# Kernel tuning notes

Measured on AMD Instinct MI355X. Metric: run time of the kernel, lower is better.

## Reference

```python
import jax, jax.numpy as jnp
import numpy as np

B, T, E = 8, 1024, 512
H = 1024            # hidden_dim
NH, QD, VD = 4, 256, 512
C1, C2 = 512, 2     # conv1_out, conv2_out
K, PAD = 3, 1


def conv1d(x, w, b, pad):
    # x: [B, Cin, T], w: [Cout, Cin, K]
    y = jax.lax.conv_general_dilated(x, w, (1,), [(pad, pad)],
                                     dimension_numbers=('NCH', 'OIH', 'NCH'))
    return y + b[None, :, None]


def setup_inputs() -> dict:
    key = jax.random.key(0)
    ks = jax.random.split(key, 24)
    n = lambda i, shape, s=0.02: jax.random.normal(ks[i], shape, dtype=jnp.float32) * s
    inp = {
        'x':    jax.random.normal(ks[0], (B, T, E), dtype=jnp.float32),
        # in_pro: two 1x1 convs over channels (acting as linears)
        'w_in1': n(1, (E, E)), 'b_in1': jnp.zeros((E,), jnp.float32),
        'w_in2': n(2, (E, E)), 'b_in2': jnp.zeros((E,), jnp.float32),
        # attention projections
        'w_q': n(3, (NH * QD, E), float(np.sqrt(2.0 / (E + QD)))), 'b_q': jnp.zeros((NH * QD,), jnp.float32),
        'w_k': n(4, (NH * QD, E), float(np.sqrt(2.0 / (E + QD)))), 'b_k': jnp.zeros((NH * QD,), jnp.float32),
        'w_v': n(5, (NH * VD, E), float(np.sqrt(2.0 / (E + VD)))), 'b_v': jnp.zeros((NH * VD,), jnp.float32),
        # output projection (1x1 conv)
        'w_p': n(6, (E, NH * VD)), 'b_p': jnp.zeros((E,), jnp.float32),
        # layernorm
        'ln_g': jnp.ones((E,), jnp.float32), 'ln_b': jnp.zeros((E,), jnp.float32),
        # LSTM (1 layer, unidirectional, hidden H)
        'w_ih': n(7, (4 * H, E)), 'w_hh': n(8, (4 * H, H)),
        'b_ih': jnp.zeros((4 * H,), jnp.float32), 'b_hh': jnp.zeros((4 * H,), jnp.float32),
        # attention pooling convs
        'w_c1': n(9, (C1, H, K)), 'b_c1': jnp.zeros((C1,), jnp.float32),
        'w_c2': n(10, (C2, C1, K)), 'b_c2': jnp.zeros((C2,), jnp.float32),
    }
    return inp


def reference(x, w_in1, b_in1, w_in2, b_in2, w_q, b_q, w_k, b_k, w_v, b_v,
              w_p, b_p, ln_g, ln_b, w_ih, w_hh, b_ih, b_hh,
              w_c1, b_c1, w_c2, b_c2):
    # in_pro: 1x1 conv -> LeakyReLU(0.25) -> 1x1 conv (channel-wise linears)
    h = jnp.einsum('bte,fe->btf', x, w_in1) + b_in1
    h = jnp.where(h >= 0, h, 0.25 * h)
    h = jnp.einsum('bte,fe->btf', h, w_in2) + b_in2  # [B,T,E]

    # multi-head attention (no scale factor, as in the source)
    q = (jnp.einsum('bte,fe->btf', h, w_q) + b_q).reshape(B, T, NH, QD)
    k = (jnp.einsum('bte,fe->btf', h, w_k) + b_k).reshape(B, T, NH, QD)
    v = (jnp.einsum('bte,fe->btf', h, w_v) + b_v).reshape(B, T, NH, VD)
    scores = jnp.einsum('btnd,bsnd->bnts', q, k)          # [B,NH,T,T]
    attn = jax.nn.softmax(scores, axis=-1)
    o = jnp.einsum('bnts,bsnd->btnd', attn, v)            # [B,T,NH,VD]
    o = o.reshape(B, T, NH * VD)

    # p_conv1 (1x1) then LayerNorm over E
    y = jnp.einsum('btc,ec->bte', o, w_p) + b_p           # [B,T,E]
    mu = jnp.mean(y, axis=-1, keepdims=True)
    var = jnp.mean(jnp.square(y - mu), axis=-1, keepdims=True)
    y = (y - mu) * jax.lax.rsqrt(var + 1e-5) * ln_g + ln_b

    # LSTM (batch_first, 1 layer); dropout is identity in eval mode
    def step(carry, xt):
        hprev, cprev = carry
        g = xt @ w_ih.T + hprev @ w_hh.T + b_ih + b_hh    # [B,4H]
        i, f, gg, og = jnp.split(g, 4, axis=-1)
        c = jax.nn.sigmoid(f) * cprev + jax.nn.sigmoid(i) * jnp.tanh(gg)
        hn = jax.nn.sigmoid(og) * jnp.tanh(c)
        return (hn, c), hn
    init = (jnp.zeros((B, H), y.dtype), jnp.zeros((B, H), y.dtype))
    _, hs = jax.lax.scan(step, init, jnp.swapaxes(y, 0, 1))  # [T,B,H]
    lstm_out = jnp.swapaxes(hs, 0, 1)                        # [B,T,H]

    # conv-based attention pooling
    a = conv1d(jnp.swapaxes(lstm_out, 1, 2), w_c1, b_c1, PAD)  # [B,C1,T]
    a = jax.nn.relu(a)
    a = conv1d(a, w_c2, b_c2, PAD)                              # [B,C2,T]
    a = jax.nn.softmax(a, axis=2)
    feat = jnp.einsum('bct,bth->bch', a, lstm_out)              # [B,C2,H]
    return feat.reshape(B, C2 * H)
```

## Files before the change

kernel.cpp:

```cpp
#include <hip/hip_runtime.h>
#include <stdint.h>

typedef short short8 __attribute__((ext_vector_type(8)));
typedef short short4v __attribute__((ext_vector_type(4)));
typedef float float4v __attribute__((ext_vector_type(4)));

__device__ __forceinline__ float b2f(short s) {
    return __uint_as_float(((unsigned)(unsigned short)s) << 16);
}
__device__ __forceinline__ short f2b(float f) {
    unsigned u = __float_as_uint(f);
    unsigned r = (u + 0x7fffu + ((u >> 16) & 1u)) >> 16;
    return (short)r;
}

__global__ void k_f32_to_bf16(const float4v* __restrict__ in, short4v* __restrict__ out, int n4) {
    int i = blockIdx.x * blockDim.x + threadIdx.x;
    int stride = gridDim.x * blockDim.x;
    for (; i < n4; i += stride) {
        float4v v = in[i];
        short4v o;
        o[0] = f2b(v[0]); o[1] = f2b(v[1]); o[2] = f2b(v[2]); o[3] = f2b(v[3]);
        out[i] = o;
    }
}

__global__ void k_cvt_weights(const float4v* __restrict__ s0, const float4v* __restrict__ s1,
                              const float4v* __restrict__ s2, const float4v* __restrict__ s3,
                              const float4v* __restrict__ s4, const float4v* __restrict__ s5,
                              const float4v* __restrict__ s6, const float4v* __restrict__ s7,
                              short4v* __restrict__ dst) {
    int i = blockIdx.x * blockDim.x + threadIdx.x;
    int stride = gridDim.x * blockDim.x;
    for (; i < 2490368; i += stride) {
        float4v v;
        if      (i <   65536) v = s0[i];
        else if (i <  131072) v = s1[i -   65536];
        else if (i <  262144) v = s2[i -  131072];
        else if (i <  393216) v = s3[i -  262144];
        else if (i <  655360) v = s4[i -  393216];
        else if (i <  917504) v = s5[i -  655360];
        else if (i < 1441792) v = s6[i -  917504];
        else                  v = s7[i - 1441792];
        short4v o;
        o[0] = f2b(v[0]); o[1] = f2b(v[1]); o[2] = f2b(v[2]); o[3] = f2b(v[3]);
        dst[i] = o;
    }
}

__global__ void k_wc1_tr(const float* __restrict__ in, short* __restrict__ out) {
    int i = blockIdx.x * blockDim.x + threadIdx.x;
    if (i >= 512 * 3072) return;
    int c = i / 3072, rr = i % 3072, dk = rr / 1024, h = rr % 1024;
    out[i] = f2b(in[(c * 1024 + h) * 3 + dk]);
}

__global__ void k_bias_sum(const float* __restrict__ a, const float* __restrict__ b,
                           float* __restrict__ o, int n) {
    int i = blockIdx.x * blockDim.x + threadIdx.x;
    if (i < n) o[i] = a[i] + b[i];
}

__global__ __launch_bounds__(256) void k_gemm_bt(
    const short* __restrict__ A, const short* __restrict__ B,
    float* __restrict__ Cf, short* __restrict__ Cb,
    const float* __restrict__ bias,
    int M, int N, int K, int lda, int ldb, int ldc,
    int z0n, long sA0, long sA1, long sB0, long sB1, long sC0, long sC1,
    int act, int gap)
{
    __shared__ __align__(16) short lds[2 * 128 * 32];
    const int z = blockIdx.z;
    const int z0 = z % z0n, z1 = z / z0n;
    A += z1 * sA1 + z0 * sA0;
    B += z1 * sB1 + z0 * sB0;
    const long coff = z1 * sC1 + z0 * sC0;
    const int tn0 = blockIdx.x * 128, tm0 = blockIdx.y * 128;
    const int tid = threadIdx.x, ln = tid & 63, wv = tid >> 6;
    const int wr = wv >> 1, wc = wv & 1;

    const short* gbase[4];
    {
        const int gcol = (ln & 3) ^ ((ln >> 3) & 3);
#pragma unroll
        for (int j = 0; j < 4; ++j) {
            int c = wv * 4 + j;
            if (c < 8) {
                long grow = (long)(tm0 + c * 16 + (ln >> 2));
                if (gap) grow += 2 * (grow >> 10);
                gbase[j] = A + grow * (long)lda + gcol * 8;
            } else {
                gbase[j] = B + (long)(tn0 + (c - 8) * 16 + (ln >> 2)) * ldb + gcol * 8;
            }
        }
    }

    float4v acc[4][4];
#pragma unroll
    for (int i = 0; i < 4; ++i)
#pragma unroll
        for (int j = 0; j < 4; ++j) acc[i][j] = (float4v){0.f, 0.f, 0.f, 0.f};

    const int nk = K >> 5;
    for (int kt = 0; kt < nk; ++kt) {
        __syncthreads();
#pragma unroll
        for (int j = 0; j < 4; ++j) {
            int c = wv * 4 + j;
            __builtin_amdgcn_global_load_lds(
                (const __attribute__((address_space(1))) void*)(gbase[j] + kt * 32),
                (__attribute__((address_space(3))) void*)((short8*)lds + c * 64),
                16, 0, 0);
        }
        __syncthreads();

        short8 af[4], bf_[4];
        const int q = ln >> 4;
#pragma unroll
        for (int i = 0; i < 4; ++i) {
            int r = wr * 64 + i * 16 + (ln & 15);
            af[i] = ((short8*)lds)[r * 4 + (q ^ ((r >> 1) & 3))];
        }
#pragma unroll
        for (int j = 0; j < 4; ++j) {
            int r = wc * 64 + j * 16 + (ln & 15);
            bf_[j] = ((short8*)lds)[512 + r * 4 + (q ^ ((r >> 1) & 3))];
        }
#pragma unroll
        for (int i = 0; i < 4; ++i)
#pragma unroll
            for (int j = 0; j < 4; ++j)
                acc[i][j] = __builtin_amdgcn_mfma_f32_16x16x32_bf16(af[i], bf_[j], acc[i][j], 0, 0, 0);
    }

#pragma unroll
    for (int j = 0; j < 4; ++j) {
        int nglob = tn0 + wc * 64 + j * 16 + (ln & 15);
        float bv = bias ? bias[nglob] : 0.f;
#pragma unroll
        for (int i = 0; i < 4; ++i) {
#pragma unroll
            for (int r = 0; r < 4; ++r) {
                int mglob = tm0 + wr * 64 + i * 16 + (ln >> 4) * 4 + r;
                float v = acc[i][j][r] + bv;
                if (act == 1) v = (v >= 0.f) ? v : 0.25f * v;
                else if (act == 2) v = fmaxf(v, 0.f);
                long ci = coff + (long)mglob * ldc + nglob;
                if (Cf) Cf[ci] = v;
                if (Cb) Cb[ci] = f2b(v);
            }
        }
    }
}

__global__ __launch_bounds__(256) void k_softmax_rows_bf16(short* __restrict__ p) {
    long row = blockIdx.x;
    short* r = p + (row << 10);
    int tid = threadIdx.x;
    float v[4];
    float mx = -3.4e38f;
#pragma unroll
    for (int i = 0; i < 4; ++i) { v[i] = b2f(r[tid + (i << 8)]); mx = fmaxf(mx, v[i]); }
#pragma unroll
    for (int d = 32; d > 0; d >>= 1) mx = fmaxf(mx, __shfl_down(mx, d));
    __shared__ float red[4], red2[4];
    if ((tid & 63) == 0) red[tid >> 6] = mx;
    __syncthreads();
    mx = fmaxf(fmaxf(red[0], red[1]), fmaxf(red[2], red[3]));
    float s = 0.f;
#pragma unroll
    for (int i = 0; i < 4; ++i) { v[i] = expf(v[i] - mx); s += v[i]; }
#pragma unroll
    for (int d = 32; d > 0; d >>= 1) s += __shfl_down(s, d);
    if ((tid & 63) == 0) red2[tid >> 6] = s;
    __syncthreads();
    s = red2[0] + red2[1] + red2[2] + red2[3];
    float inv = 1.f / s;
#pragma unroll
    for (int i = 0; i < 4; ++i) r[tid + (i << 8)] = f2b(v[i] * inv);
}

__global__ __launch_bounds__(256) void k_layernorm(const short* __restrict__ y,
                                                   const float* __restrict__ gam,
                                                   const float* __restrict__ bet,
                                                   short* __restrict__ o) {
    const long row = blockIdx.x;
    const short* r = y + (row << 9);
    const int tid = threadIdx.x;
    float v0 = b2f(r[tid]), v1 = b2f(r[tid + 256]);
    float s = v0 + v1, ss = v0 * v0 + v1 * v1;
#pragma unroll
    for (int d = 32; d > 0; d >>= 1) { s += __shfl_down(s, d); ss += __shfl_down(ss, d); }
    __shared__ float rs_[4], rss[4];
    if ((tid & 63) == 0) { rs_[tid >> 6] = s; rss[tid >> 6] = ss; }
    __syncthreads();
    s = rs_[0] + rs_[1] + rs_[2] + rs_[3];
    ss = rss[0] + rss[1] + rss[2] + rss[3];
    float mean = s * (1.f / 512.f);
    float var = ss * (1.f / 512.f) - mean * mean;
    float rstd = rsqrtf(var + 1e-5f);
    short* out = o + (row << 9);
    out[tid]       = f2b((v0 - mean) * rstd * gam[tid]       + bet[tid]);
    out[tid + 256] = f2b((v1 - mean) * rstd * gam[tid + 256] + bet[tid + 256]);
}

__global__ __launch_bounds__(256) void k_vT(const short* __restrict__ v, short* __restrict__ vT) {
    __shared__ short t[32][34];
    int bn = blockIdx.z, b = bn >> 2, n = bn & 3;
    int s0 = blockIdx.y * 32, d0 = blockIdx.x * 32;
    int lx = threadIdx.x & 31, ly = threadIdx.x >> 5;
#pragma unroll
    for (int i = 0; i < 4; ++i) {
        int s = ly + i * 8;
        t[s][lx] = v[(long)(b * 1024 + s0 + s) * 2048 + n * 512 + d0 + lx];
    }
    __syncthreads();
#pragma unroll
    for (int i = 0; i < 4; ++i) {
        int d = ly + i * 8;
        vT[((long)bn * 512 + d0 + d) * 1024 + s0 + lx] = t[lx][d];
    }
}

__global__ __launch_bounds__(256) void k_lstm(
    const short* __restrict__ whh, const short* __restrict__ igb,
    short* __restrict__ hA, short* __restrict__ hB,
    short* __restrict__ lstm_pad, int* __restrict__ arr)
{
    const int g = blockIdx.x;
    const int tid = threadIdx.x;
    const int ln = tid & 63, wv = tid >> 6;
    const int kbase = wv * 256 + ((ln >> 4) << 3);
    const int arow = ln & 15;

    short8 wf[4][8];
#pragma unroll
    for (int q = 0; q < 4; ++q) {
        long row = (long)q * 1024 + g * 16 + (ln & 15);
#pragma unroll
        for (int kk = 0; kk < 8; ++kk)
            wf[q][kk] = *(const short8*)&whh[row * 1024 + kbase + kk * 32];
    }

    __shared__ float part[4][16][68];
    const int gm = tid >> 4, gu = tid & 15;
    float c_prev = 0.f;
    float igv[4];
    if (tid < 128) {
#pragma unroll
        for (int q = 0; q < 4; ++q)
            igv[q] = b2f(igb[((long)gm * 1024 + 0) * 4096 + q * 1024 + g * 16 + gu]);
    }

    for (int step = 0; step < 1024; ++step) {
        const short* hp = (step & 1) ? hB : hA;
        short8 af[8];
        if (arow < 8) {
            const unsigned long long* hq =
                (const unsigned long long*)(hp + arow * 1024 + kbase);
#pragma unroll
            for (int kk = 0; kk < 8; ++kk) {
                union { unsigned long long u[2]; short8 s; } cv;
                cv.u[0] = __hip_atomic_load(hq + kk * 8,     __ATOMIC_RELAXED, __HIP_MEMORY_SCOPE_AGENT);
                cv.u[1] = __hip_atomic_load(hq + kk * 8 + 1, __ATOMIC_RELAXED, __HIP_MEMORY_SCOPE_AGENT);
                af[kk] = cv.s;
            }
        } else {
#pragma unroll
            for (int kk = 0; kk < 8; ++kk) af[kk] = (short8){0, 0, 0, 0, 0, 0, 0, 0};
        }

        float4v acc[4];
#pragma unroll
        for (int q = 0; q < 4; ++q) acc[q] = (float4v){0.f, 0.f, 0.f, 0.f};
#pragma unroll
        for (int kk = 0; kk < 8; ++kk)
#pragma unroll
            for (int q = 0; q < 4; ++q)
                acc[q] = __builtin_amdgcn_mfma_f32_16x16x32_bf16(af[kk], wf[q][kk], acc[q], 0, 0, 0);

#pragma unroll
        for (int q = 0; q < 4; ++q)
#pragma unroll
            for (int rr = 0; rr < 4; ++rr)
                part[wv][(ln >> 4) * 4 + rr][q * 16 + (ln & 15)] = acc[q][rr];
        __syncthreads();

        if (tid < 128) {
            float psum[4];
#pragma unroll
            for (int q = 0; q < 4; ++q)
                psum[q] = part[0][gm][q * 16 + gu] + part[1][gm][q * 16 + gu]
                        + part[2][gm][q * 16 + gu] + part[3][gm][q * 16 + gu];
            float g0 = psum[0] + igv[0];
            float g1 = psum[1] + igv[1];
            float g2 = psum[2] + igv[2];
            float g3 = psum[3] + igv[3];
            float iv = 1.f / (1.f + __expf(-g0));
            float fv = 1.f / (1.f + __expf(-g1));
            float gv = 2.f / (1.f + __expf(-2.f * g2)) - 1.f;
            float ov = 1.f / (1.f + __expf(-g3));
            float c = fv * c_prev + iv * gv;
            c_prev = c;
            float h = ov * (2.f / (1.f + __expf(-2.f * c)) - 1.f);
            short hb16 = f2b(h);
            short* hn = (step & 1) ? hA : hB;
            __hip_atomic_store(&hn[gm * 1024 + g * 16 + gu], hb16,
                               __ATOMIC_RELAXED, __HIP_MEMORY_SCOPE_AGENT);
            lstm_pad[((long)gm * 1026 + step + 1) * 1024 + g * 16 + gu] = hb16;
        }

        __syncthreads();
        if (tid == 0)
            __hip_atomic_store(&arr[g], step + 1, __ATOMIC_RELAXED, __HIP_MEMORY_SCOPE_AGENT);
        if (tid < 128 && step + 1 < 1024) {
#pragma unroll
            for (int q = 0; q < 4; ++q)
                igv[q] = b2f(igb[((long)gm * 1024 + step + 1) * 4096 + q * 1024 + g * 16 + gu]);
        }
        if (wv == 0) {
            const int target = step + 1;
            long att = 0;
            while (true) {
                int f0 = __hip_atomic_load(&arr[ln], __ATOMIC_RELAXED, __HIP_MEMORY_SCOPE_AGENT);
                if (__all(f0 >= target)) break;
                if (++att > 20000000L) break;
                __builtin_amdgcn_s_sleep(1);
            }
        }
        __syncthreads();
    }
}

__global__ __launch_bounds__(256) void k_conv2(const short* __restrict__ a1,
                                               const float* __restrict__ w,
                                               const float* __restrict__ bias,
                                               float* __restrict__ a2) {
    __shared__ float wl[1536];
    int blk = blockIdx.x;
    int b = blk >> 3, c = (blk >> 2) & 1, t0 = (blk & 3) * 256;
    int tid = threadIdx.x;
    for (int i = tid; i < 1536; i += 256) wl[i] = w[c * 1536 + i];
    __syncthreads();
    int t = t0 + tid;
    float s = bias[c];
    for (int dk = 0; dk < 3; ++dk) {
        int tt = t + dk - 1;
        if (tt < 0 || tt >= 1024) continue;
        const short8* arow = (const short8*)(a1 + (long)(b * 1024 + tt) * 512);
        for (int j = 0; j < 64; ++j) {
            short8 v = arow[j];
#pragma unroll
            for (int u = 0; u < 8; ++u)
                s += b2f(v[u]) * wl[(j * 8 + u) * 3 + dk];
        }
    }
    a2[(b * 2 + c) * 1024 + t] = s;
}

__global__ __launch_bounds__(256) void k_feat(const float* __restrict__ a2,
                                              const short* __restrict__ lstm_pad,
                                              float* __restrict__ out) {
    int blk = blockIdx.x;
    int bc = blk >> 2, qh = blk & 3;
    int b = bc >> 1;
    int tid = threadIdx.x;
    int h = qh * 256 + tid;
    __shared__ float aw[1024];
    __shared__ float red[4], red2[4];
    float v[4];
    float mx = -3.4e38f;
#pragma unroll
    for (int i = 0; i < 4; ++i) { v[i] = a2[bc * 1024 + tid + (i << 8)]; mx = fmaxf(mx, v[i]); }
#pragma unroll
    for (int d = 32; d > 0; d >>= 1) mx = fmaxf(mx, __shfl_down(mx, d));
    if ((tid & 63) == 0) red[tid >> 6] = mx;
    __syncthreads();
    mx = fmaxf(fmaxf(red[0], red[1]), fmaxf(red[2], red[3]));
    float s = 0.f;
#pragma unroll
    for (int i = 0; i < 4; ++i) { v[i] = __expf(v[i] - mx); s += v[i]; }
#pragma unroll
    for (int d = 32; d > 0; d >>= 1) s += __shfl_down(s, d);
    if ((tid & 63) == 0) red2[tid >> 6] = s;
    __syncthreads();
    s = red2[0] + red2[1] + red2[2] + red2[3];
    float inv = 1.f / s;
#pragma unroll
    for (int i = 0; i < 4; ++i) aw[tid + (i << 8)] = v[i] * inv;
    __syncthreads();
    float acc = 0.f;
#pragma unroll 4
    for (int t = 0; t < 1024; ++t)
        acc += aw[t] * b2f(lstm_pad[((long)(b * 1026 + t + 1)) * 1024 + h]);
    out[bc * 1024 + h] = acc;
}

static void gemm_bt(hipStream_t st, const short* A, const short* B, float* Cf, short* Cb,
                    const float* bias, int M, int N, int K, int lda, int ldb, int ldc,
                    int z, int z0n, long sA0, long sA1, long sB0, long sB1, long sC0, long sC1,
                    int act, int gap) {
    dim3 grid(N / 128, M / 128, z);
    k_gemm_bt<<<grid, dim3(256), 0, st>>>(A, B, Cf, Cb, bias, M, N, K, lda, ldb, ldc,
                                          z0n, sA0, sA1, sB0, sB1, sC0, sC1, act, gap);
}

extern "C" void kernel_launch(void* const* d_in, const int* in_sizes, int n_in,
                              void* d_out, int out_size, void* d_ws, size_t ws_size,
                              hipStream_t stream) {
    if (ws_size < 199409920u) return;

    const float* x     = (const float*)d_in[0];
    const float* w_in1 = (const float*)d_in[1];
    const float* b_in1 = (const float*)d_in[2];
    const float* w_in2 = (const float*)d_in[3];
    const float* b_in2 = (const float*)d_in[4];
    const float* w_q   = (const float*)d_in[5];
    const float* b_q   = (const float*)d_in[6];
    const float* w_k   = (const float*)d_in[7];
    const float* b_k   = (const float*)d_in[8];
    const float* w_v   = (const float*)d_in[9];
    const float* b_v   = (const float*)d_in[10];
    const float* w_p   = (const float*)d_in[11];
    const float* b_p   = (const float*)d_in[12];
    const float* ln_g  = (const float*)d_in[13];
    const float* ln_b  = (const float*)d_in[14];
    const float* w_ih  = (const float*)d_in[15];
    const float* w_hh  = (const float*)d_in[16];
    const float* b_ih  = (const float*)d_in[17];
    const float* b_hh  = (const float*)d_in[18];
    const float* w_c1  = (const float*)d_in[19];
    const float* b_c1  = (const float*)d_in[20];
    const float* w_c2  = (const float*)d_in[21];
    const float* b_c2  = (const float*)d_in[22];

    char* ws = (char*)d_ws;
    short* w1b  = (short*)(ws + 0);
    short* w2b  = (short*)(ws + 524288);
    short* wqb  = (short*)(ws + 1048576);
    short* wkb  = (short*)(ws + 2097152);
    short* wvb  = (short*)(ws + 3145728);
    short* wpb  = (short*)(ws + 5242880);
    short* wihb = (short*)(ws + 7340032);
    short* whhb = (short*)(ws + 11534336);
    short* wc1b = (short*)(ws + 19922944);
    float* bsum = (float*)(ws + 23068672);
    short* hs0  = (short*)(ws + 23085056);
    short* hs1  = (short*)(ws + 23117824);
    int*   arr  = (int*)  (ws + 23150592);
    float* a2   = (float*)(ws + 23150848);
    short* lpad = (short*)(ws + 23216384);
    const size_t D0 = 40026368u;
    short* xbf   = (short*)(ws + D0);
    short* h1bf  = (short*)(ws + D0 + 8388608);
    short* h2bf  = (short*)(ws + D0 + 16777216);
    short* qbf   = (short*)(ws + D0 + 25165824);
    short* kbf   = (short*)(ws + D0 + 41943040);
    short* vbf   = (short*)(ws + D0 + 58720256);
    short* vTbf  = (short*)(ws + D0 + 92274688);
    short* scb   = (short*)(ws + D0 + 58720256);
    short* obf   = (short*)(ws + D0 + 125829120);
    short* ybf   = (short*)(ws + D0 + 58720256);
    short* ylnbf = (short*)(ws + D0 + 67108864);
    short* igb   = (short*)(ws + D0 + 92274688);
    short* a1bf  = (short*)(ws + D0);

    hipMemsetAsync(lpad, 0, (size_t)8 * 1026 * 1024 * 2, stream);
    hipMemsetAsync(hs0, 0, 32768, stream);
    hipMemsetAsync(hs1, 0, 32768, stream);
    hipMemsetAsync(arr, 0, 512, stream);

    k_f32_to_bf16<<<dim3(4096), dim3(256), 0, stream>>>((const float4v*)x, (short4v*)xbf, 1048576);
    k_cvt_weights<<<dim3(4096), dim3(256), 0, stream>>>(
        (const float4v*)w_in1, (const float4v*)w_in2, (const float4v*)w_q, (const float4v*)w_k,
        (const float4v*)w_v, (const float4v*)w_p, (const float4v*)w_ih, (const float4v*)w_hh,
        (short4v*)w1b);
    k_wc1_tr<<<dim3((512 * 3072 + 255) / 256), dim3(256), 0, stream>>>(w_c1, wc1b);
    k_bias_sum<<<dim3(16), dim3(256), 0, stream>>>(b_ih, b_hh, bsum, 4096);

    gemm_bt(stream, xbf, w1b, nullptr, h1bf, b_in1, 8192, 512, 512, 512, 512, 512,
            1, 1, 0, 0, 0, 0, 0, 0, 1, 0);
    gemm_bt(stream, h1bf, w2b, nullptr, h2bf, b_in2, 8192, 512, 512, 512, 512, 512,
            1, 1, 0, 0, 0, 0, 0, 0, 0, 0);
    gemm_bt(stream, h2bf, wqb, nullptr, qbf, b_q, 8192, 1024, 512, 512, 512, 1024,
            1, 1, 0, 0, 0, 0, 0, 0, 0, 0);
    gemm_bt(stream, h2bf, wkb, nullptr, kbf, b_k, 8192, 1024, 512, 512, 512, 1024,
            1, 1, 0, 0, 0, 0, 0, 0, 0, 0);
    gemm_bt(stream, h2bf, wvb, nullptr, vbf, b_v, 8192, 2048, 512, 512, 512, 2048,
            1, 1, 0, 0, 0, 0, 0, 0, 0, 0);
    k_vT<<<dim3(16, 32, 32), dim3(256), 0, stream>>>(vbf, vTbf);

    for (int bg = 0; bg < 2; ++bg) {
        const short* qb = qbf + (long)bg * 4194304;
        const short* kb = kbf + (long)bg * 4194304;
        gemm_bt(stream, qb, kb, nullptr, scb, nullptr, 1024, 1024, 256, 1024, 1024, 1024,
                16, 4, 256, 1048576, 256, 1048576, 1048576, 4194304, 0, 0);
        k_softmax_rows_bf16<<<dim3(16384), dim3(256), 0, stream>>>(scb);
        gemm_bt(stream, scb, vTbf + (long)bg * 8388608, nullptr, obf + (long)bg * 8388608, nullptr,
                1024, 512, 1024, 1024, 1024, 2048,
                16, 4, 1048576, 4194304, 524288, 2097152, 512, 2097152, 0, 0);
    }

    gemm_bt(stream, obf, wpb, nullptr, ybf, b_p, 8192, 512, 2048, 2048, 2048, 512,
            1, 1, 0, 0, 0, 0, 0, 0, 0, 0);
    k_layernorm<<<dim3(8192), dim3(256), 0, stream>>>(ybf, ln_g, ln_b, ylnbf);
    gemm_bt(stream, ylnbf, wihb, nullptr, igb, bsum, 8192, 4096, 512, 512, 512, 4096,
            1, 1, 0, 0, 0, 0, 0, 0, 0, 0);
    k_lstm<<<dim3(64), dim3(256), 0, stream>>>(whhb, igb, hs0, hs1, lpad, arr);
    gemm_bt(stream, lpad, wc1b, nullptr, a1bf, b_c1, 8192, 512, 3072, 1024, 3072, 512,
            1, 1, 0, 0, 0, 0, 0, 0, 2, 1);
    k_conv2<<<dim3(64), dim3(256), 0, stream>>>(a1bf, w_c2, b_c2, a2);
    k_feat<<<dim3(64), dim3(256), 0, stream>>>(a2, lpad, (float*)d_out);
    (void)in_sizes; (void)n_in; (void)out_size; (void)ws_size;
}
```

Before: 4.042 ms.

## Replace LSTM cross-block flag barrier with step-tagged hidden-state words

The persistent LSTM kernel previously published the hidden state, ran a block barrier, set a per-block arrival flag, and spun until all 64 flags reached the step. Each bf16 hidden value is now stored in a 32-bit word together with a 16-bit step tag. Consumers poll the hidden-state loads directly until every tag matches, which removes the arrival array, one __syncthreads, and the separate flag spin per step. This doubles the hidden-state buffer traffic and makes every wave spin on wider atomic loads without sleeping, which adds memory pressure while blocks wait.

```diff
diff --git a/kernel.cpp b/kernel.cpp
--- a/kernel.cpp
+++ b/kernel.cpp
@@ -224,8 +224,8 @@
 
 __global__ __launch_bounds__(256) void k_lstm(
     const short* __restrict__ whh, const short* __restrict__ igb,
-    short* __restrict__ hA, short* __restrict__ hB,
-    short* __restrict__ lstm_pad, int* __restrict__ arr)
+    unsigned* __restrict__ hA, unsigned* __restrict__ hB,
+    short* __restrict__ lstm_pad)
 {
     const int g = blockIdx.x;
     const int tid = threadIdx.x;
@@ -253,19 +253,39 @@
     }
 
     for (int step = 0; step < 1024; ++step) {
-        const short* hp = (step & 1) ? hB : hA;
+        const unsigned* hp = (step & 1) ? hB : hA;
         short8 af[8];
-        if (arow < 8) {
-            const unsigned long long* hq =
-                (const unsigned long long*)(hp + arow * 1024 + kbase);
-#pragma unroll
-            for (int kk = 0; kk < 8; ++kk) {
-                union { unsigned long long u[2]; short8 s; } cv;
-                cv.u[0] = __hip_atomic_load(hq + kk * 8,     __ATOMIC_RELAXED, __HIP_MEMORY_SCOPE_AGENT);
-                cv.u[1] = __hip_atomic_load(hq + kk * 8 + 1, __ATOMIC_RELAXED, __HIP_MEMORY_SCOPE_AGENT);
-                af[kk] = cv.s;
+        const unsigned long long tagw = (unsigned long long)((unsigned)step & 0xffffu);
+        const unsigned long long tagpair = tagw | (tagw << 32);
+        const unsigned long long tmask = 0x0000ffff0000ffffULL;
+        const unsigned long long* hq =
+            (const unsigned long long*)(hp + (arow & 7) * 1024 + kbase);
+
+        long att = 0;
+        bool done = false;
+        while (!done) {
+            bool ok = true;
+            if (arow < 8) {
+#pragma unroll
+                for (int kk = 0; kk < 8; ++kk) {
+                    unsigned long long u0 = __hip_atomic_load(hq + kk * 16 + 0, __ATOMIC_RELAXED, __HIP_MEMORY_SCOPE_AGENT);
+                    unsigned long long u1 = __hip_atomic_load(hq + kk * 16 + 1, __ATOMIC_RELAXED, __HIP_MEMORY_SCOPE_AGENT);
+                    unsigned long long u2 = __hip_atomic_load(hq + kk * 16 + 2, __ATOMIC_RELAXED, __HIP_MEMORY_SCOPE_AGENT);
+                    unsigned long long u3 = __hip_atomic_load(hq + kk * 16 + 3, __ATOMIC_RELAXED, __HIP_MEMORY_SCOPE_AGENT);
+                    ok = ok & ((u0 & tmask) == tagpair) & ((u1 & tmask) == tagpair)
+                            & ((u2 & tmask) == tagpair) & ((u3 & tmask) == tagpair);
+                    union { unsigned u[4]; short8 s; } cv;
+                    cv.u[0] = (((unsigned)(u0 >> 16)) & 0xffffu) | (((unsigned)(u0 >> 48)) << 16);
+                    cv.u[1] = (((unsigned)(u1 >> 16)) & 0xffffu) | (((unsigned)(u1 >> 48)) << 16);
+                    cv.u[2] = (((unsigned)(u2 >> 16)) & 0xffffu) | (((unsigned)(u2 >> 48)) << 16);
+                    cv.u[3] = (((unsigned)(u3 >> 16)) & 0xffffu) | (((unsigned)(u3 >> 48)) << 16);
+                    af[kk] = cv.s;
+                }
             }
-        } else {
+            done = __all(ok);
+            if (++att > 20000000L) break;
+        }
+        if (arow >= 8) {
 #pragma unroll
             for (int kk = 0; kk < 8; ++kk) af[kk] = (short8){0, 0, 0, 0, 0, 0, 0, 0};
         }
@@ -304,29 +324,18 @@
             c_prev = c;
             float h = ov * (2.f / (1.f + __expf(-2.f * c)) - 1.f);
             short hb16 = f2b(h);
-            short* hn = (step & 1) ? hA : hB;
-            __hip_atomic_store(&hn[gm * 1024 + g * 16 + gu], hb16,
+            unsigned* hn = (step & 1) ? hA : hB;
+            unsigned pw = (((unsigned)(unsigned short)hb16) << 16)
+                        | ((unsigned)(step + 1) & 0xffffu);
+            __hip_atomic_store(&hn[gm * 1024 + g * 16 + gu], pw,
                                __ATOMIC_RELAXED, __HIP_MEMORY_SCOPE_AGENT);
             lstm_pad[((long)gm * 1026 + step + 1) * 1024 + g * 16 + gu] = hb16;
         }
 
-        __syncthreads();
-        if (tid == 0)
-            __hip_atomic_store(&arr[g], step + 1, __ATOMIC_RELAXED, __HIP_MEMORY_SCOPE_AGENT);
         if (tid < 128 && step + 1 < 1024) {
 #pragma unroll
             for (int q = 0; q < 4; ++q)
                 igv[q] = b2f(igb[((long)gm * 1024 + step + 1) * 4096 + q * 1024 + g * 16 + gu]);
-        }
-        if (wv == 0) {
-            const int target = step + 1;
-            long att = 0;
-            while (true) {
-                int f0 = __hip_atomic_load(&arr[ln], __ATOMIC_RELAXED, __HIP_MEMORY_SCOPE_AGENT);
-                if (__all(f0 >= target)) break;
-                if (++att > 20000000L) break;
-                __builtin_amdgcn_s_sleep(1);
-            }
         }
         __syncthreads();
     }
@@ -445,9 +454,8 @@
     short* whhb = (short*)(ws + 11534336);
     short* wc1b = (short*)(ws + 19922944);
     float* bsum = (float*)(ws + 23068672);
-    short* hs0  = (short*)(ws + 23085056);
-    short* hs1  = (short*)(ws + 23117824);
-    int*   arr  = (int*)  (ws + 23150592);
+    unsigned* hs0 = (unsigned*)(ws + 23085056);
+    unsigned* hs1 = (unsigned*)(ws + 23117824);
     float* a2   = (float*)(ws + 23150848);
     short* lpad = (short*)(ws + 23216384);
     const size_t D0 = 40026368u;
@@ -468,7 +476,6 @@
     hipMemsetAsync(lpad, 0, (size_t)8 * 1026 * 1024 * 2, stream);
     hipMemsetAsync(hs0, 0, 32768, stream);
     hipMemsetAsync(hs1, 0, 32768, stream);
-    hipMemsetAsync(arr, 0, 512, stream);
 
     k_f32_to_bf16<<<dim3(4096), dim3(256), 0, stream>>>((const float4v*)x, (short4v*)xbf, 1048576);
     k_cvt_weights<<<dim3(4096), dim3(256), 0, stream>>>(
@@ -506,7 +513,7 @@
     k_layernorm<<<dim3(8192), dim3(256), 0, stream>>>(ybf, ln_g, ln_b, ylnbf);
     gemm_bt(stream, ylnbf, wihb, nullptr, igb, bsum, 8192, 4096, 512, 512, 512, 4096,
             1, 1, 0, 0, 0, 0, 0, 0, 0, 0);
-    k_lstm<<<dim3(64), dim3(256), 0, stream>>>(whhb, igb, hs0, hs1, lpad, arr);
+    k_lstm<<<dim3(64), dim3(256), 0, stream>>>(whhb, igb, hs0, hs1, lpad);
     gemm_bt(stream, lpad, wc1b, nullptr, a1bf, b_c1, 8192, 512, 3072, 1024, 3072, 512,
             1, 1, 0, 0, 0, 0, 0, 0, 2, 1);
     k_conv2<<<dim3(64), dim3(256), 0, stream>>>(a1bf, w_c2, b_c2, a2);
```

Result: slower. 5.908 ms (+46.2%).

## Fold LSTM cell update into one wave and drop a barrier per step

Applied to the files above, without the earlier changes.

The pointwise LSTM cell update moves from 128 threads to a single wave where each lane handles two hidden units and uses packed 32-bit loads and stores. The same wave waits for its stores to finish and then publishes the arrival flag, so the second __syncthreads per step is gone. A different wave now spins on the grid-wide flags, which lets flag publication and polling overlap. This shortens the serial critical path of the 1024-step recurrence, but it concentrates more transcendental work on one wave and relies on the vmcnt wait to order the flag after the h stores.

```diff
diff --git a/kernel.cpp b/kernel.cpp
--- a/kernel.cpp
+++ b/kernel.cpp
@@ -243,13 +243,17 @@
     }
 
     __shared__ float part[4][16][68];
-    const int gm = tid >> 4, gu = tid & 15;
-    float c_prev = 0.f;
-    float igv[4];
-    if (tid < 128) {
-#pragma unroll
-        for (int q = 0; q < 4; ++q)
-            igv[q] = b2f(igb[((long)gm * 1024 + 0) * 4096 + q * 1024 + g * 16 + gu]);
+    const int gm = ln >> 3;
+    const int u0 = (ln & 7) * 2;
+    float c0 = 0.f, c1 = 0.f;
+    float ig0[4], ig1[4];
+    if (wv == 0) {
+#pragma unroll
+        for (int q = 0; q < 4; ++q) {
+            unsigned iv = *(const unsigned*)&igb[((long)gm * 1024 + 0) * 4096 + q * 1024 + g * 16 + u0];
+            ig0[q] = b2f((short)(iv & 0xffffu));
+            ig1[q] = b2f((short)(iv >> 16));
+        }
     }
 
     for (int step = 0; step < 1024; ++step) {
@@ -286,44 +290,51 @@
                 part[wv][(ln >> 4) * 4 + rr][q * 16 + (ln & 15)] = acc[q][rr];
         __syncthreads();
 
-        if (tid < 128) {
-            float psum[4];
-#pragma unroll
-            for (int q = 0; q < 4; ++q)
-                psum[q] = part[0][gm][q * 16 + gu] + part[1][gm][q * 16 + gu]
-                        + part[2][gm][q * 16 + gu] + part[3][gm][q * 16 + gu];
-            float g0 = psum[0] + igv[0];
-            float g1 = psum[1] + igv[1];
-            float g2 = psum[2] + igv[2];
-            float g3 = psum[3] + igv[3];
-            float iv = 1.f / (1.f + __expf(-g0));
-            float fv = 1.f / (1.f + __expf(-g1));
-            float gv = 2.f / (1.f + __expf(-2.f * g2)) - 1.f;
-            float ov = 1.f / (1.f + __expf(-g3));
-            float c = fv * c_prev + iv * gv;
-            c_prev = c;
-            float h = ov * (2.f / (1.f + __expf(-2.f * c)) - 1.f);
-            short hb16 = f2b(h);
+        if (wv == 0) {
+            float gg0[4], gg1[4];
+#pragma unroll
+            for (int q = 0; q < 4; ++q) {
+                float s0 = 0.f, s1 = 0.f;
+#pragma unroll
+                for (int w = 0; w < 4; ++w) {
+                    s0 += part[w][gm][q * 16 + u0];
+                    s1 += part[w][gm][q * 16 + u0 + 1];
+                }
+                gg0[q] = s0 + ig0[q];
+                gg1[q] = s1 + ig1[q];
+            }
+            float i0 = 1.f / (1.f + __expf(-gg0[0])), i1 = 1.f / (1.f + __expf(-gg1[0]));
+            float f0 = 1.f / (1.f + __expf(-gg0[1])), f1 = 1.f / (1.f + __expf(-gg1[1]));
+            float z0 = 2.f / (1.f + __expf(-2.f * gg0[2])) - 1.f;
+            float z1 = 2.f / (1.f + __expf(-2.f * gg1[2])) - 1.f;
+            float o0 = 1.f / (1.f + __expf(-gg0[3])), o1 = 1.f / (1.f + __expf(-gg1[3]));
+            c0 = f0 * c0 + i0 * z0;
+            c1 = f1 * c1 + i1 * z1;
+            float h0 = o0 * (2.f / (1.f + __expf(-2.f * c0)) - 1.f);
+            float h1 = o1 * (2.f / (1.f + __expf(-2.f * c1)) - 1.f);
+            unsigned hw = (unsigned)(unsigned short)f2b(h0)
+                        | ((unsigned)(unsigned short)f2b(h1) << 16);
             short* hn = (step & 1) ? hA : hB;
-            __hip_atomic_store(&hn[gm * 1024 + g * 16 + gu], hb16,
+            __hip_atomic_store((unsigned*)&hn[gm * 1024 + g * 16 + u0], hw,
                                __ATOMIC_RELAXED, __HIP_MEMORY_SCOPE_AGENT);
-            lstm_pad[((long)gm * 1026 + step + 1) * 1024 + g * 16 + gu] = hb16;
-        }
-
-        __syncthreads();
-        if (tid == 0)
-            __hip_atomic_store(&arr[g], step + 1, __ATOMIC_RELAXED, __HIP_MEMORY_SCOPE_AGENT);
-        if (tid < 128 && step + 1 < 1024) {
-#pragma unroll
-            for (int q = 0; q < 4; ++q)
-                igv[q] = b2f(igb[((long)gm * 1024 + step + 1) * 4096 + q * 1024 + g * 16 + gu]);
-        }
-        if (wv == 0) {
+            asm volatile("s_waitcnt vmcnt(0)" ::: "memory");
+            if (ln == 0)
+                __hip_atomic_store(&arr[g], step + 1, __ATOMIC_RELAXED, __HIP_MEMORY_SCOPE_AGENT);
+            *(unsigned*)&lstm_pad[((long)gm * 1026 + step + 1) * 1024 + g * 16 + u0] = hw;
+            if (step + 1 < 1024) {
+#pragma unroll
+                for (int q = 0; q < 4; ++q) {
+                    unsigned iv = *(const unsigned*)&igb[((long)gm * 1024 + step + 1) * 4096 + q * 1024 + g * 16 + u0];
+                    ig0[q] = b2f((short)(iv & 0xffffu));
+                    ig1[q] = b2f((short)(iv >> 16));
+                }
+            }
+        } else if (wv == 1 && step + 1 < 1024) {
             const int target = step + 1;
             long att = 0;
             while (true) {
-                int f0 = __hip_atomic_load(&arr[ln], __ATOMIC_RELAXED, __HIP_MEMORY_SCOPE_AGENT);
-                if (__all(f0 >= target)) break;
+                int f = __hip_atomic_load(&arr[ln], __ATOMIC_RELAXED, __HIP_MEMORY_SCOPE_AGENT);
+                if (__all(f >= target)) break;
                 if (++att > 20000000L) break;
                 __builtin_amdgcn_s_sleep(1);
             }
```

Result: slower. 5.371 ms (+32.9%).
